# Kernel optimization log

Hardware: AMD Instinct MI355X
Metric: run time of the kernel (lower is better)

Reference implementation:

```python
import jax, jax.numpy as jnp
import numpy as np

N_ETYPES = 4


def setup_inputs() -> dict:
    key = jax.random.key(0)
    ks = jax.random.split(key, 6)
    N, E, F = 50000, 800000, 128
    x = jax.random.normal(ks[0], (N, F), dtype=jnp.float32)
    edge_index = jax.random.randint(ks[1], (2, E), 0, N, dtype=jnp.int64)
    edge_type = jax.random.randint(ks[2], (E,), 0, N_ETYPES, dtype=jnp.int64)
    scale = 1.0 / np.sqrt(F)
    W_self = jax.random.normal(ks[3], (N_ETYPES, F, F), dtype=jnp.float32) * scale
    W_neigh = jax.random.normal(ks[4], (N_ETYPES, F, F), dtype=jnp.float32) * scale
    b = jnp.zeros((N_ETYPES, F), dtype=jnp.float32)
    return {"x": x, "edge_index": edge_index, "edge_type": edge_type,
            "W_self": W_self, "W_neigh": W_neigh, "b": b}


def reference(x, edge_index, edge_type, W_self, W_neigh, b):
    # HeteroConv: per-edge-type SageConv (mean aggregation), then mean over types.
    N = x.shape[0]
    src, dst = edge_index[0], edge_index[1]
    msg = x[src]                                   # [E, F] gathered source features
    outs = []
    for t in range(N_ETYPES):                      # small fixed loop over edge types
        w = (edge_type == t).astype(x.dtype)[:, None]          # [E, 1] type mask
        agg = jax.ops.segment_sum(msg * w, dst, num_segments=N)  # [N, F]
        cnt = jax.ops.segment_sum(w, dst, num_segments=N)        # [N, 1]
        mean_agg = agg / jnp.maximum(cnt, 1.0)
        outs.append(x @ W_self[t] + mean_agg @ W_neigh[t] + b[t])
    out = jnp.stack(outs, axis=0)                  # [n_etypes, N, F]
    return out.mean(axis=0)                        # reduction='mean' over edge types
```

## Files before the change

### kernel.cpp

```cpp
#include <hip/hip_runtime.h>

#define FDIM 128
#define NT 4
#define KDIM (FDIM * (NT + 1))
#define GBM 64

#define RSH 6
#define RNODES 64
#define RCAP 1280
#define NBKT 256
#define CHUNK 4096

typedef __attribute__((ext_vector_type(8))) _Float16 h8v;
typedef __attribute__((ext_vector_type(4))) float f4v;

__device__ __forceinline__ unsigned short f2h(float f) {
    _Float16 h = (_Float16)f;
    return __builtin_bit_cast(unsigned short, h);
}
__device__ __forceinline__ void gload_lds16(const void* g, void* l) {
    __builtin_amdgcn_global_load_lds(
        (const __attribute__((address_space(1))) unsigned int*)g,
        (__attribute__((address_space(3))) unsigned int*)l, 16, 0, 0);
}

__global__ __launch_bounds__(256) void x2h(const float* __restrict__ x,
                                           unsigned short* __restrict__ xh, int n4) {
    int i = blockIdx.x * blockDim.x + threadIdx.x;
    if (i < n4) {
        float4 v = reinterpret_cast<const float4*>(x)[i];
        ushort4 o;
        o.x = f2h(v.x);
        o.y = f2h(v.y);
        o.z = f2h(v.z);
        o.w = f2h(v.w);
        reinterpret_cast<ushort4*>(xh)[i] = o;
    }
}

__global__ void mix_weights(const float* __restrict__ Wself,
                            const float* __restrict__ Wneigh,
                            const float* __restrict__ b,
                            unsigned short* __restrict__ WmixT,
                            float* __restrict__ bmean) {
    int i = blockIdx.x * blockDim.x + threadIdx.x;
    if (i >= KDIM * FDIM) return;
    int k = i / FDIM, j = i % FDIM;
    float v;
    if (k < FDIM) {
        v = 0.25f * (Wself[(size_t)(0 * FDIM + k) * FDIM + j] +
                     Wself[(size_t)(1 * FDIM + k) * FDIM + j] +
                     Wself[(size_t)(2 * FDIM + k) * FDIM + j] +
                     Wself[(size_t)(3 * FDIM + k) * FDIM + j]);
    } else {
        int t = (k - FDIM) >> 7;
        int kk = (k - FDIM) & (FDIM - 1);
        v = 0.25f * Wneigh[((size_t)t * FDIM + kk) * FDIM + j];
    }
    WmixT[(size_t)j * KDIM + k] = f2h(v);
    if (i < FDIM) {
        bmean[i] = 0.25f * (b[i] + b[FDIM + i] + b[2 * FDIM + i] + b[3 * FDIM + i]);
    }
}

__global__ __launch_bounds__(256) void k_bin(
    const int* __restrict__ ei, const int* __restrict__ et,
    int* __restrict__ cur, unsigned int* __restrict__ bin,
    int N, int E, int NR) {
    __shared__ int lcnt[1024];
    __shared__ int lpos[1024];
    const int tid = threadIdx.x;
    const int e0 = blockIdx.x * CHUNK;

    for (int b = tid; b < NR; b += 256) lcnt[b] = 0;
    __syncthreads();

    int rs[16];
    unsigned int recs[16];
#pragma unroll
    for (int i = 0; i < 16; ++i) {
        int e = e0 + i * 256 + tid;
        if (e < E) {
            int src = ei[e];
            int dst = ei[E + e];
            int t = et[e];
            rs[i] = dst >> RSH;
            recs[i] = (unsigned int)src |
                      ((unsigned int)(dst & (RNODES - 1)) << 16) |
                      ((unsigned int)t << 22);
            atomicAdd(&lcnt[rs[i]], 1);
        } else {
            rs[i] = -1;
            recs[i] = 0;
        }
    }
    __syncthreads();

    for (int b = tid; b < NR; b += 256) {
        int c = lcnt[b];
        lpos[b] = (c > 0) ? atomicAdd(&cur[b * 16], c) : 0;
    }
    __syncthreads();

#pragma unroll
    for (int i = 0; i < 16; ++i) {
        if (rs[i] >= 0) {
            int p = atomicAdd(&lpos[rs[i]], 1);
            if (p < RCAP) bin[(size_t)rs[i] * RCAP + p] = recs[i];
        }
    }
}

__global__ __launch_bounds__(256) void k_aggb(
    const unsigned short* __restrict__ xh, const int* __restrict__ cur,
    const unsigned int* __restrict__ bin, unsigned short* __restrict__ maggh,
    int N) {
    __shared__ unsigned int recs[RCAP];
    __shared__ unsigned short srcs[RCAP];
    __shared__ int cnts[NBKT];
    __shared__ int scanb[NBKT];
    __shared__ int boff[NBKT];
    __shared__ int cur2[NBKT];

    const int r = blockIdx.x;
    const int tid = threadIdx.x;
    int K = cur[r * 16];
    if (K > RCAP) K = RCAP;

    for (int i = tid; i < K; i += 256) recs[i] = bin[(size_t)r * RCAP + i];
    cnts[tid] = 0;
    __syncthreads();
    for (int i = tid; i < K; i += 256) {
        unsigned int rec = recs[i];
        int b = ((rec >> 22) << 6) | ((rec >> 16) & 63);
        atomicAdd(&cnts[b], 1);
    }
    __syncthreads();
    int v = cnts[tid];
    scanb[tid] = v;
    __syncthreads();
    for (int off = 1; off < NBKT; off <<= 1) {
        int tv = (tid >= off) ? scanb[tid - off] : 0;
        __syncthreads();
        scanb[tid] += tv;
        __syncthreads();
    }
    boff[tid] = scanb[tid] - v;
    cur2[tid] = scanb[tid] - v;
    __syncthreads();
    for (int i = tid; i < K; i += 256) {
        unsigned int rec = recs[i];
        int b = ((rec >> 22) << 6) | ((rec >> 16) & 63);
        int p = atomicAdd(&cur2[b], 1);
        srcs[p] = (unsigned short)(rec & 0xffffu);
    }
    __syncthreads();

    const int g = tid >> 4, ln = tid & 15;
#pragma unroll 1
    for (int it = 0; it < 16; ++it) {
        int b = it * 16 + g;
        int dl = b & 63, ty = b >> 6;
        int dst = (r << RSH) + dl;
        if (dst >= N) continue;
        int beg = boff[b], m = cnts[b];
        h8v a = (h8v)(_Float16)0.f;
        h8v bb = (h8v)(_Float16)0.f;
        int i = 0;
        for (; i + 2 <= m; i += 2) {
            int s0 = srcs[beg + i];
            int s1 = srcs[beg + i + 1];
            h8v v0 = *reinterpret_cast<const h8v*>(xh + (size_t)s0 * FDIM + ln * 8);
            h8v v1 = *reinterpret_cast<const h8v*>(xh + (size_t)s1 * FDIM + ln * 8);
            a += v0;
            bb += v1;
        }
        if (i < m) {
            int s0 = srcs[beg + i];
            a += *reinterpret_cast<const h8v*>(xh + (size_t)s0 * FDIM + ln * 8);
        }
        float rc = (m > 0) ? 1.0f / (float)m : 0.0f;
        h8v o = (a + bb) * (_Float16)rc;
        *reinterpret_cast<h8v*>(maggh + ((size_t)ty * N + dst) * FDIM + ln * 8) = o;
    }
}

__global__ __launch_bounds__(256) void gemm_mfma(
    const unsigned short* __restrict__ xh, const unsigned short* __restrict__ maggh,
    const unsigned short* __restrict__ WmixT, const float* __restrict__ bmean,
    float* __restrict__ out, int M) {
    __shared__ unsigned short As[GBM * 32];
    __shared__ unsigned short Bs[FDIM * 32];

    const int tid = threadIdx.x;
    const int wid = tid >> 6, lane = tid & 63;
    const int wr = wid >> 1, wc = wid & 1;
    const int n0 = blockIdx.x * GBM;
    const int r16 = lane & 15, kg = lane >> 4;

    f4v acc[2][4];
#pragma unroll
    for (int m = 0; m < 2; ++m)
#pragma unroll
        for (int n = 0; n < 4; ++n) acc[m][n] = (f4v){0.f, 0.f, 0.f, 0.f};

    for (int k0 = 0; k0 < KDIM; k0 += 32) {
        {
            int row = tid >> 2, c = tid & 3;
            int cs = c ^ ((row >> 1) & 3);
            int rg = n0 + row; if (rg >= M) rg = M - 1;
            int seg = k0 >> 7, kc = k0 & 127;
            const unsigned short* g = (seg == 0)
                ? (xh + (size_t)rg * FDIM + kc + cs * 8)
                : (maggh + ((size_t)(seg - 1) * M + rg) * FDIM + kc + cs * 8);
            gload_lds16(g, &As[wid * 512]);
        }
#pragma unroll
        for (int p = 0; p < 2; ++p) {
            int ck = p * 256 + tid;
            int col = ck >> 2, c = ck & 3;
            int cs = c ^ ((col >> 1) & 3);
            const unsigned short* g = WmixT + (size_t)col * KDIM + k0 + cs * 8;
            gload_lds16(g, &Bs[(p * 4 + wid) * 512]);
        }
        __syncthreads();

        h8v af[2], bfr[4];
#pragma unroll
        for (int m = 0; m < 2; ++m) {
            int row = wr * 32 + m * 16 + r16;
            af[m] = *reinterpret_cast<const h8v*>(
                &As[row * 32 + ((kg ^ ((row >> 1) & 3)) << 3)]);
        }
#pragma unroll
        for (int n = 0; n < 4; ++n) {
            int col = wc * 64 + n * 16 + r16;
            bfr[n] = *reinterpret_cast<const h8v*>(
                &Bs[col * 32 + ((kg ^ ((col >> 1) & 3)) << 3)]);
        }
#pragma unroll
        for (int m = 0; m < 2; ++m)
#pragma unroll
            for (int n = 0; n < 4; ++n)
                acc[m][n] = __builtin_amdgcn_mfma_f32_16x16x32_f16(
                    af[m], bfr[n], acc[m][n], 0, 0, 0);
        __syncthreads();
    }

    float bm[4];
#pragma unroll
    for (int n = 0; n < 4; ++n) bm[n] = bmean[wc * 64 + n * 16 + r16];
#pragma unroll
    for (int m = 0; m < 2; ++m) {
#pragma unroll
        for (int j = 0; j < 4; ++j) {
            int row = n0 + wr * 32 + m * 16 + kg * 4 + j;
            if (row < M) {
                float* o = out + (size_t)row * FDIM;
#pragma unroll
                for (int n = 0; n < 4; ++n)
                    o[wc * 64 + n * 16 + r16] = acc[m][n][j] + bm[n];
            }
        }
    }
}

extern "C" void kernel_launch(void* const* d_in, const int* in_sizes, int n_in,
                              void* d_out, int out_size, void* d_ws, size_t ws_size,
                              hipStream_t stream) {
    const float* x      = (const float*)d_in[0];
    const int*   ei     = (const int*)d_in[1];
    const int*   et     = (const int*)d_in[2];
    const float* Wself  = (const float*)d_in[3];
    const float* Wneigh = (const float*)d_in[4];
    const float* b      = (const float*)d_in[5];
    float* out = (float*)d_out;

    const int N = in_sizes[0] / FDIM;
    const int E = in_sizes[2];
    const int NB = NT * N;
    const int NR = (N + RNODES - 1) >> RSH;

    char* ws = (char*)d_ws;
    unsigned short* maggh = (unsigned short*)ws;
    unsigned short* xh    = maggh + (size_t)NB * FDIM;
    unsigned short* WmixT = xh + (size_t)N * FDIM;
    float* bmean = (float*)(WmixT + (size_t)FDIM * KDIM);
    int* cur     = (int*)(bmean + FDIM);
    unsigned int* bin = (unsigned int*)(cur + (size_t)NR * 16);

    hipMemsetAsync(cur, 0, (size_t)NR * 16 * sizeof(int), stream);

    x2h<<<(N * FDIM / 4 + 255) / 256, 256, 0, stream>>>(x, xh, N * FDIM / 4);

    mix_weights<<<(KDIM * FDIM + 255) / 256, 256, 0, stream>>>(Wself, Wneigh, b, WmixT, bmean);

    k_bin<<<(E + CHUNK - 1) / CHUNK, 256, 0, stream>>>(ei, et, cur, bin, N, E, NR);

    k_aggb<<<NR, 256, 0, stream>>>(xh, cur, bin, maggh, N);

    gemm_mfma<<<(N + GBM - 1) / GBM, 256, 0, stream>>>(xh, maggh, WmixT, bmean, out, N);
}
```

Measured before the change: 100.2 us.

## Fuse neighbor aggregation into the MFMA GEMM, keeping aggregates in LDS

Merges the per-bucket mean aggregation kernel and the GEMM kernel into one kernel per 64-node block. The self-feature GEMM runs first, then each edge type's aggregate is computed into a swizzled LDS tile and immediately multiplied against the matching weight slice. This removes the global write and re-read of the fp16 aggregated features and one kernel launch. In exchange, per-block LDS use grows and the latency-bound gathers are serialized with the MFMA phases inside a block, which may lower occupancy.

```diff
diff --git a/kernel.cpp b/kernel.cpp
--- a/kernel.cpp
+++ b/kernel.cpp
@@ -111,22 +111,25 @@
     }
 }
 
-__global__ __launch_bounds__(256) void k_aggb(
+__global__ __launch_bounds__(256) void k_fused(
     const unsigned short* __restrict__ xh, const int* __restrict__ cur,
-    const unsigned int* __restrict__ bin, unsigned short* __restrict__ maggh,
-    int N) {
+    const unsigned int* __restrict__ bin, const unsigned short* __restrict__ WmixT,
+    const float* __restrict__ bmean, float* __restrict__ out, int N) {
     __shared__ unsigned int recs[RCAP];
     __shared__ unsigned short srcs[RCAP];
     __shared__ int cnts[NBKT];
     __shared__ int scanb[NBKT];
     __shared__ int boff[NBKT];
     __shared__ int cur2[NBKT];
+    __shared__ unsigned short magg[RNODES * FDIM];
+    __shared__ unsigned short As[GBM * 32];
+    __shared__ unsigned short Bs[FDIM * 32];
 
     const int r = blockIdx.x;
     const int tid = threadIdx.x;
+
     int K = cur[r * 16];
     if (K > RCAP) K = RCAP;
-
     for (int i = tid; i < K; i += 256) recs[i] = bin[(size_t)r * RCAP + i];
     cnts[tid] = 0;
     __syncthreads();
@@ -154,77 +157,38 @@
         int p = atomicAdd(&cur2[b], 1);
         srcs[p] = (unsigned short)(rec & 0xffffu);
     }
-    __syncthreads();
-
-    const int g = tid >> 4, ln = tid & 15;
-#pragma unroll 1
-    for (int it = 0; it < 16; ++it) {
-        int b = it * 16 + g;
-        int dl = b & 63, ty = b >> 6;
-        int dst = (r << RSH) + dl;
-        if (dst >= N) continue;
-        int beg = boff[b], m = cnts[b];
-        h8v a = (h8v)(_Float16)0.f;
-        h8v bb = (h8v)(_Float16)0.f;
-        int i = 0;
-        for (; i + 2 <= m; i += 2) {
-            int s0 = srcs[beg + i];
-            int s1 = srcs[beg + i + 1];
-            h8v v0 = *reinterpret_cast<const h8v*>(xh + (size_t)s0 * FDIM + ln * 8);
-            h8v v1 = *reinterpret_cast<const h8v*>(xh + (size_t)s1 * FDIM + ln * 8);
-            a += v0;
-            bb += v1;
-        }
-        if (i < m) {
-            int s0 = srcs[beg + i];
-            a += *reinterpret_cast<const h8v*>(xh + (size_t)s0 * FDIM + ln * 8);
-        }
-        float rc = (m > 0) ? 1.0f / (float)m : 0.0f;
-        h8v o = (a + bb) * (_Float16)rc;
-        *reinterpret_cast<h8v*>(maggh + ((size_t)ty * N + dst) * FDIM + ln * 8) = o;
-    }
-}
-
-__global__ __launch_bounds__(256) void gemm_mfma(
-    const unsigned short* __restrict__ xh, const unsigned short* __restrict__ maggh,
-    const unsigned short* __restrict__ WmixT, const float* __restrict__ bmean,
-    float* __restrict__ out, int M) {
-    __shared__ unsigned short As[GBM * 32];
-    __shared__ unsigned short Bs[FDIM * 32];
-
-    const int tid = threadIdx.x;
+
     const int wid = tid >> 6, lane = tid & 63;
     const int wr = wid >> 1, wc = wid & 1;
-    const int n0 = blockIdx.x * GBM;
+    const int n0 = r * GBM;
     const int r16 = lane & 15, kg = lane >> 4;
+    const int g = tid >> 4, ln = tid & 15;
 
     f4v acc[2][4];
 #pragma unroll
     for (int m = 0; m < 2; ++m)
 #pragma unroll
         for (int n = 0; n < 4; ++n) acc[m][n] = (f4v){0.f, 0.f, 0.f, 0.f};
-
-    for (int k0 = 0; k0 < KDIM; k0 += 32) {
+    __syncthreads();
+
+#pragma unroll 1
+    for (int ks = 0; ks < 4; ++ks) {
+        int k0 = ks * 32;
         {
             int row = tid >> 2, c = tid & 3;
             int cs = c ^ ((row >> 1) & 3);
-            int rg = n0 + row; if (rg >= M) rg = M - 1;
-            int seg = k0 >> 7, kc = k0 & 127;
-            const unsigned short* g = (seg == 0)
-                ? (xh + (size_t)rg * FDIM + kc + cs * 8)
-                : (maggh + ((size_t)(seg - 1) * M + rg) * FDIM + kc + cs * 8);
-            gload_lds16(g, &As[wid * 512]);
+            int rg = n0 + row; if (rg >= N) rg = N - 1;
+            gload_lds16(xh + (size_t)rg * FDIM + k0 + cs * 8, &As[wid * 512]);
         }
 #pragma unroll
         for (int p = 0; p < 2; ++p) {
             int ck = p * 256 + tid;
             int col = ck >> 2, c = ck & 3;
             int cs = c ^ ((col >> 1) & 3);
-            const unsigned short* g = WmixT + (size_t)col * KDIM + k0 + cs * 8;
-            gload_lds16(g, &Bs[(p * 4 + wid) * 512]);
-        }
-        __syncthreads();
-
+            gload_lds16(WmixT + (size_t)col * KDIM + k0 + cs * 8,
+                        &Bs[(p * 4 + wid) * 512]);
+        }
+        __syncthreads();
         h8v af[2], bfr[4];
 #pragma unroll
         for (int m = 0; m < 2; ++m) {
@@ -247,6 +211,67 @@
         __syncthreads();
     }
 
+#pragma unroll 1
+    for (int t = 0; t < 4; ++t) {
+#pragma unroll 1
+        for (int it = 0; it < 4; ++it) {
+            int dl = it * 16 + g;
+            int b = (t << 6) | dl;
+            int beg = boff[b], m = cnts[b];
+            h8v a = (h8v)(_Float16)0.f;
+            h8v bb = (h8v)(_Float16)0.f;
+            int i = 0;
+            for (; i + 2 <= m; i += 2) {
+                int s0 = srcs[beg + i];
+                int s1 = srcs[beg + i + 1];
+                a  += *reinterpret_cast<const h8v*>(xh + (size_t)s0 * FDIM + ln * 8);
+                bb += *reinterpret_cast<const h8v*>(xh + (size_t)s1 * FDIM + ln * 8);
+            }
+            if (i < m) {
+                int s0 = srcs[beg + i];
+                a += *reinterpret_cast<const h8v*>(xh + (size_t)s0 * FDIM + ln * 8);
+            }
+            float rc = (m > 0) ? 1.0f / (float)m : 0.0f;
+            h8v o = (a + bb) * (_Float16)rc;
+            *reinterpret_cast<h8v*>(&magg[dl * FDIM + ((ln ^ (dl & 15)) << 3)]) = o;
+        }
+        __syncthreads();
+
+#pragma unroll 1
+        for (int ks = 0; ks < 4; ++ks) {
+            int k0 = FDIM + t * FDIM + ks * 32;
+#pragma unroll
+            for (int p = 0; p < 2; ++p) {
+                int ck = p * 256 + tid;
+                int col = ck >> 2, c = ck & 3;
+                int cs = c ^ ((col >> 1) & 3);
+                gload_lds16(WmixT + (size_t)col * KDIM + k0 + cs * 8,
+                            &Bs[(p * 4 + wid) * 512]);
+            }
+            __syncthreads();
+            h8v af[2], bfr[4];
+#pragma unroll
+            for (int m = 0; m < 2; ++m) {
+                int row = wr * 32 + m * 16 + r16;
+                af[m] = *reinterpret_cast<const h8v*>(
+                    &magg[row * FDIM + (((ks * 4 + kg) ^ (row & 15)) << 3)]);
+            }
+#pragma unroll
+            for (int n = 0; n < 4; ++n) {
+                int col = wc * 64 + n * 16 + r16;
+                bfr[n] = *reinterpret_cast<const h8v*>(
+                    &Bs[col * 32 + ((kg ^ ((col >> 1) & 3)) << 3)]);
+            }
+#pragma unroll
+            for (int m = 0; m < 2; ++m)
+#pragma unroll
+                for (int n = 0; n < 4; ++n)
+                    acc[m][n] = __builtin_amdgcn_mfma_f32_16x16x32_f16(
+                        af[m], bfr[n], acc[m][n], 0, 0, 0);
+            __syncthreads();
+        }
+    }
+
     float bm[4];
 #pragma unroll
     for (int n = 0; n < 4; ++n) bm[n] = bmean[wc * 64 + n * 16 + r16];
@@ -255,7 +280,7 @@
 #pragma unroll
         for (int j = 0; j < 4; ++j) {
             int row = n0 + wr * 32 + m * 16 + kg * 4 + j;
-            if (row < M) {
+            if (row < N) {
                 float* o = out + (size_t)row * FDIM;
 #pragma unroll
                 for (int n = 0; n < 4; ++n)
@@ -278,12 +303,10 @@
 
     const int N = in_sizes[0] / FDIM;
     const int E = in_sizes[2];
-    const int NB = NT * N;
     const int NR = (N + RNODES - 1) >> RSH;
 
     char* ws = (char*)d_ws;
-    unsigned short* maggh = (unsigned short*)ws;
-    unsigned short* xh    = maggh + (size_t)NB * FDIM;
+    unsigned short* xh    = (unsigned short*)ws;
     unsigned short* WmixT = xh + (size_t)N * FDIM;
     float* bmean = (float*)(WmixT + (size_t)FDIM * KDIM);
     int* cur     = (int*)(bmean + FDIM);
@@ -297,7 +320,5 @@
 
     k_bin<<<(E + CHUNK - 1) / CHUNK, 256, 0, stream>>>(ei, et, cur, bin, N, E, NR);
 
-    k_aggb<<<NR, 256, 0, stream>>>(xh, cur, bin, maggh, N);
-
-    gemm_mfma<<<(N + GBM - 1) / GBM, 256, 0, stream>>>(xh, maggh, WmixT, bmean, out, N);
-}
+    k_fused<<<NR, 256, 0, stream>>>(xh, cur, bin, WmixT, bmean, out, N);
+}
```

Measured after the change: 91.03 us. 1.1x faster.
